# Performance work log

Measured on AMD Instinct MI355X. Metric: run time of the kernel, lower is better.

Reference implementation:

```python
import jax, jax.numpy as jnp
import numpy as np

D = 64          # cfg.D_PAIR
NT = 6          # cfg.N_TORSION_OUT
LN_EPS = 1e-5


def _layernorm(x, g, b):
    # torch LayerNorm computed in float32 then cast back
    x32 = x.astype(jnp.float32)
    m = jnp.mean(x32, axis=-1, keepdims=True)
    v = jnp.var(x32, axis=-1, keepdims=True)
    y = (x32 - m) / jnp.sqrt(v + LN_EPS) * g + b
    return y.astype(x.dtype)


def setup_inputs() -> dict:
    key = jax.random.key(0)
    ks = jax.random.split(key, 16)
    B, L = 2, 512
    s = 0.125  # ~xavier scale for fan 64
    inp = {
        "pair": jax.random.normal(ks[0], (B, L, L, D), jnp.float32),
        "torsion": jax.random.normal(ks[1], (B, L, NT), jnp.float32),
        "ln_g": jnp.ones((D,), jnp.float32),
        "ln_b": jnp.zeros((D,), jnp.float32),
        "Wl": jax.random.normal(ks[2], (D, D), jnp.float32) * s,
        "Wr": jax.random.normal(ks[3], (D, D), jnp.float32) * s,
        "Wlg": jax.random.normal(ks[4], (D, D), jnp.float32) * s,
        "blg": jnp.zeros((D,), jnp.float32),
        "Wrg": jax.random.normal(ks[5], (D, D), jnp.float32) * s,
        "brg": jnp.zeros((D,), jnp.float32),
        "Wog": jax.random.normal(ks[6], (D, D), jnp.float32) * s,
        "bog": jnp.zeros((D,), jnp.float32),
        "Wout": jax.random.normal(ks[7], (D, D), jnp.float32) * s,  # 'final' init is zeros; randomized to exercise math
        "bout": jnp.zeros((D,), jnp.float32),
        "lno_g": jnp.ones((D,), jnp.float32),
        "lno_b": jnp.zeros((D,), jnp.float32),
        "Wt": jax.random.normal(ks[8], (1, NT), jnp.float32) * 0.4,
        "bt": jnp.zeros((1,), jnp.float32),
    }
    return inp


def reference(pair, torsion, ln_g, ln_b, Wl, Wr, Wlg, blg, Wrg, brg,
              Wog, bog, Wout, bout, lno_g, lno_b, Wt, bt):
    B, L, _, d = pair.shape
    z = _layernorm(pair, ln_g, ln_b)                         # [B,L,L,D]
    a = (z @ Wl.T) * jax.nn.sigmoid(z @ Wlg.T + blg)         # left proj * gate
    b = (z @ Wr.T) * jax.nn.sigmoid(z @ Wrg.T + brg)         # right proj * gate
    t_w = jax.nn.sigmoid(torsion @ Wt.T + bt)[..., 0]        # [B,L]
    # outgoing=True branch: tw unsqueezed to [B,1,L,1] then transposed(1,2) -> [B,L,1,1]
    a_w = a * t_w[:, :, None, None]
    x = jnp.einsum('bikd,bjkd->bijd', a_w, b) / (L ** 0.5 + 1e-8)
    g = jax.nn.sigmoid(z @ Wog.T + bog)
    out = (_layernorm(x, lno_g, lno_b) @ Wout.T + bout) * g
    return pair + out
```

## Files before the change

kernel.cpp:

```cpp
#include <hip/hip_runtime.h>
#include <stdint.h>

#define LL 512
#define DD 64

typedef __attribute__((ext_vector_type(8))) short bf16x8;
typedef __attribute__((ext_vector_type(4))) float f32x4;

#define MFMA16(a, b, c) __builtin_amdgcn_mfma_f32_16x16x32_bf16((a), (b), (c), 0, 0, 0)

__device__ __forceinline__ float bf2f(unsigned short u) {
    union { unsigned int i; float f; } v; v.i = ((unsigned int)u) << 16; return v.f;
}
__device__ __forceinline__ unsigned short f2bf(float f) {
    union { float f; unsigned int i; } v; v.f = f;
    unsigned int i = v.i;
    return (unsigned short)((i + 0x7FFFu + ((i >> 16) & 1u)) >> 16);
}
__device__ __forceinline__ float sigm(float x) {
    float d = 1.0f + __expf(-x);
    float y = __builtin_amdgcn_rcpf(d);
    return y * __builtin_fmaf(-d, y, 2.0f);
}

__global__ void prep_w(const float* __restrict__ Wl, const float* __restrict__ Wr,
                       const float* __restrict__ Wlg, const float* __restrict__ Wrg,
                       const float* __restrict__ Wog, const float* __restrict__ Wout,
                       unsigned short* __restrict__ Wcat, unsigned short* __restrict__ WoutB) {
    int t = threadIdx.x + blockIdx.x * blockDim.x;
    int stride = blockDim.x * gridDim.x;
    for (int idx = t; idx < 320 * 64; idx += stride) {
        int row = idx >> 6, col = idx & 63;
        int sec = row >> 6, r = row & 63;
        float v;
        switch (sec) {
            case 0:  v = Wl[r * 64 + col];  break;
            case 1:  v = Wlg[r * 64 + col]; break;
            case 2:  v = Wr[r * 64 + col];  break;
            case 3:  v = Wrg[r * 64 + col]; break;
            default: v = Wog[r * 64 + col]; break;
        }
        Wcat[idx] = f2bf(v);
    }
    for (int idx = t; idx < 64 * 64; idx += stride) WoutB[idx] = f2bf(Wout[idx]);
}

__launch_bounds__(256)
__global__ void k1_proj(const float* __restrict__ pair, const float* __restrict__ torsion,
                        const float* __restrict__ ln_g, const float* __restrict__ ln_b,
                        const float* __restrict__ blg, const float* __restrict__ brg,
                        const float* __restrict__ bog, const float* __restrict__ Wt,
                        const float* __restrict__ bt, const unsigned short* __restrict__ Wcat,
                        unsigned short* __restrict__ At, unsigned short* __restrict__ Bt,
                        unsigned short* __restrict__ G) {
    const int bb = blockIdx.z, irow = blockIdx.y, c0 = blockIdx.x * 128;
    const int t = threadIdx.x, w = t >> 6, lane = t & 63;
    const int rsel = lane & 15, koff = lane >> 4;
    const int col = w * 16 + rsel;
    __shared__ unsigned short zs[128][72];
    __shared__ unsigned short awL[64][132];
    __shared__ unsigned short bL[64][132];

    float tww;
    {
        float acc = bt[0];
        #pragma unroll
        for (int n = 0; n < 6; ++n) acc += torsion[(bb * LL + irow) * 6 + n] * Wt[n];
        tww = sigm(acc);
    }

    bf16x8 wfr[5][2];
    #pragma unroll
    for (int s = 0; s < 5; ++s)
        #pragma unroll
        for (int kh = 0; kh < 2; ++kh)
            wfr[s][kh] = *(const bf16x8*)&Wcat[(size_t)(s * 64 + col) * 64 + kh * 32 + koff * 8];
    const float vblg = blg[col], vbrg = brg[col], vbog = bog[col];

    {
        const int sub = lane & 3, rr = lane >> 2;
        const float4* pr4 = (const float4*)(pair + ((size_t)(bb * LL + irow) * LL + c0) * DD);
        #pragma unroll
        for (int p = 0; p < 2; ++p) {
            const int row = w * 32 + p * 16 + rr;
            float4 x[4];
            #pragma unroll
            for (int q = 0; q < 4; ++q) x[q] = pr4[row * 16 + sub * 4 + q];
            float s = 0.f, s2 = 0.f;
            #pragma unroll
            for (int q = 0; q < 4; ++q) {
                s += x[q].x + x[q].y + x[q].z + x[q].w;
                s2 += x[q].x * x[q].x + x[q].y * x[q].y + x[q].z * x[q].z + x[q].w * x[q].w;
            }
            s += __shfl_xor(s, 1);  s2 += __shfl_xor(s2, 1);
            s += __shfl_xor(s, 2);  s2 += __shfl_xor(s2, 2);
            float m = s * 0.015625f;
            float var = s2 * 0.015625f - m * m;
            float rstd = rsqrtf(var + 1e-5f);
            #pragma unroll
            for (int q = 0; q < 4; ++q) {
                float4 lg4 = ((const float4*)ln_g)[sub * 4 + q];
                float4 lb4 = ((const float4*)ln_b)[sub * 4 + q];
                ushort4 zw;
                zw.x = f2bf((x[q].x - m) * rstd * lg4.x + lb4.x);
                zw.y = f2bf((x[q].y - m) * rstd * lg4.y + lb4.y);
                zw.z = f2bf((x[q].z - m) * rstd * lg4.z + lb4.z);
                zw.w = f2bf((x[q].w - m) * rstd * lg4.w + lb4.w);
                *(ushort4*)&zs[row][sub * 16 + q * 4] = zw;
            }
        }
    }
    __syncthreads();

    ushort4 gk[8];
    #pragma unroll
    for (int mi = 0; mi < 8; ++mi) {
        bf16x8 a0 = *(const bf16x8*)&zs[mi * 16 + rsel][koff * 8];
        bf16x8 a1 = *(const bf16x8*)&zs[mi * 16 + rsel][32 + koff * 8];
        f32x4 pl = {0.f, 0.f, 0.f, 0.f}, plg = pl, pr = pl, prg = pl, pog = pl;
        pl  = MFMA16(a0, wfr[0][0], pl);  pl  = MFMA16(a1, wfr[0][1], pl);
        plg = MFMA16(a0, wfr[1][0], plg); plg = MFMA16(a1, wfr[1][1], plg);
        pr  = MFMA16(a0, wfr[2][0], pr);  pr  = MFMA16(a1, wfr[2][1], pr);
        prg = MFMA16(a0, wfr[3][0], prg); prg = MFMA16(a1, wfr[3][1], prg);
        pog = MFMA16(a0, wfr[4][0], pog); pog = MFMA16(a1, wfr[4][1], pog);

        const int crow = mi * 16 + koff * 4;
        unsigned short aw4[4], bm4[4], g4[4];
        #pragma unroll
        for (int r = 0; r < 4; ++r) {
            float av = pl[r] * sigm(plg[r] + vblg) * tww;
            float bv = pr[r] * sigm(prg[r] + vbrg);
            float gv = sigm(pog[r] + vbog);
            aw4[r] = f2bf(av); bm4[r] = f2bf(bv); g4[r] = f2bf(gv);
        }
        *(ushort4*)&awL[col][crow] = make_ushort4(aw4[0], aw4[1], aw4[2], aw4[3]);
        *(ushort4*)&bL[col][crow]  = make_ushort4(bm4[0], bm4[1], bm4[2], bm4[3]);
        gk[mi] = make_ushort4(g4[0], g4[1], g4[2], g4[3]);
    }
    __syncthreads();

    #pragma unroll
    for (int mi = 0; mi < 8; ++mi) {
        const int rbase = mi * 16 + koff * 4;
        zs[rbase + 0][col] = gk[mi].x;
        zs[rbase + 1][col] = gk[mi].y;
        zs[rbase + 2][col] = gk[mi].z;
        zs[rbase + 3][col] = gk[mi].w;
    }
    __syncthreads();

    #pragma unroll
    for (int it = 0; it < 8; ++it) {
        int d = it * 8 + (t >> 5);
        int c8 = (t & 31) * 4;
        size_t base = ((size_t)(bb * 64 + d) * LL + irow) * LL + c0 + c8;
        *(ushort4*)&At[base] = *(const ushort4*)&awL[d][c8];
        *(ushort4*)&Bt[base] = *(const ushort4*)&bL[d][c8];
    }
    #pragma unroll
    for (int it = 0; it < 8; ++it) {
        int r = it * 16 + (t >> 4), cc = (t & 15) * 4;
        size_t pos = (size_t)(bb * LL + irow) * LL + c0 + r;
        *(ushort4*)&G[pos * DD + cc] = *(const ushort4*)&zs[r][cc];
    }
}

__launch_bounds__(256, 2)
__global__ void k2_gemm(const unsigned short* __restrict__ At,
                        const unsigned short* __restrict__ Bt,
                        unsigned short* __restrict__ Xt) {
    int lin = blockIdx.x + (blockIdx.y << 4);
    int nlin = (lin & 7) * 256 + (lin >> 3);
    const int p = nlin >> 4;
    const int tile = nlin & 15;
    const int i0 = (tile >> 2) * 128, j0 = (tile & 3) * 128;
    const int t = threadIdx.x, lane = t & 63, w = t >> 6;
    const int wm = w >> 1, wn = w & 1;
    const int rsel = lane & 15, koff = lane >> 4;
    __shared__ unsigned short Cs[128][136];

    f32x4 acc[4][4];
    #pragma unroll
    for (int i = 0; i < 4; ++i)
        #pragma unroll
        for (int j = 0; j < 4; ++j) acc[i][j] = (f32x4){0.f, 0.f, 0.f, 0.f};

    const unsigned short* ap =
        At + (size_t)p * LL * LL + (size_t)(i0 + wm * 64 + rsel) * LL + koff * 8;
    const unsigned short* bp =
        Bt + (size_t)p * LL * LL + (size_t)(j0 + wn * 64 + rsel) * LL + koff * 8;

    for (int k0 = 0; k0 < LL; k0 += 32) {
        bf16x8 af[4], bfr[4];
        #pragma unroll
        for (int mi = 0; mi < 4; ++mi)
            af[mi] = *(const bf16x8*)(ap + (size_t)mi * 16 * LL + k0);
        #pragma unroll
        for (int ni = 0; ni < 4; ++ni)
            bfr[ni] = *(const bf16x8*)(bp + (size_t)ni * 16 * LL + k0);
        #pragma unroll
        for (int mi = 0; mi < 4; ++mi)
            #pragma unroll
            for (int ni = 0; ni < 4; ++ni)
                acc[mi][ni] = MFMA16(af[mi], bfr[ni], acc[mi][ni]);
    }

    const float s = 1.0f / (sqrtf((float)LL) + 1e-8f);
    #pragma unroll
    for (int mi = 0; mi < 4; ++mi)
        #pragma unroll
        for (int ni = 0; ni < 4; ++ni)
            #pragma unroll
            for (int r = 0; r < 4; ++r)
                Cs[wm * 64 + mi * 16 + koff * 4 + r][wn * 64 + ni * 16 + rsel] =
                    f2bf(acc[mi][ni][r] * s);
    __syncthreads();
    #pragma unroll
    for (int it = 0; it < 8; ++it) {
        int row = it * 16 + (t >> 4), colc = (t & 15) * 8;
        uint4 v = *(const uint4*)&Cs[row][colc];
        *(uint4*)&Xt[((size_t)p * LL + i0 + row) * LL + j0 + colc] = v;
    }
}

__launch_bounds__(256)
__global__ void k3_out(const unsigned short* __restrict__ Xt, const unsigned short* __restrict__ G,
                       const float* __restrict__ pairIn, const unsigned short* __restrict__ WoutB,
                       const float* __restrict__ lno_g, const float* __restrict__ lno_b,
                       const float* __restrict__ bout, float* __restrict__ out) {
    const int bb = blockIdx.z, irow = blockIdx.y, c0 = blockIdx.x * 128;
    const int t = threadIdx.x, w = t >> 6, lane = t & 63;
    __shared__ unsigned short x1[64][128];
    __shared__ unsigned short x2[128][72];

    #pragma unroll
    for (int q = 0; q < 4; ++q) {
        int idx = t + q * 256, d = idx >> 4, c8 = idx & 15;
        uint4 v = *(const uint4*)&Xt[((size_t)(bb * 64 + d) * LL + irow) * LL + c0 + c8 * 8];
        *(uint4*)&x1[d][c8 * 8] = v;
    }
    __syncthreads();
    {
        const int c = t & 127, half = t >> 7;
        unsigned short tmp[32];
        #pragma unroll
        for (int dd = 0; dd < 32; ++dd) tmp[dd] = x1[half * 32 + dd][c];
        #pragma unroll
        for (int q = 0; q < 4; ++q)
            *(uint4*)&x2[c][half * 32 + q * 8] = *(const uint4*)&tmp[q * 8];
    }
    __syncthreads();

    {
        const int sub = lane & 3, rr = lane >> 2;
        #pragma unroll
        for (int p = 0; p < 2; ++p) {
            const int row = w * 32 + p * 16 + rr;
            ushort4 raw[4];
            #pragma unroll
            for (int q = 0; q < 4; ++q) raw[q] = *(const ushort4*)&x2[row][sub * 16 + q * 4];
            float xv[16];
            #pragma unroll
            for (int q = 0; q < 4; ++q) {
                xv[q * 4 + 0] = bf2f(raw[q].x);
                xv[q * 4 + 1] = bf2f(raw[q].y);
                xv[q * 4 + 2] = bf2f(raw[q].z);
                xv[q * 4 + 3] = bf2f(raw[q].w);
            }
            float s = 0.f, s2 = 0.f;
            #pragma unroll
            for (int e = 0; e < 16; ++e) { s += xv[e]; s2 += xv[e] * xv[e]; }
            s += __shfl_xor(s, 1);  s2 += __shfl_xor(s2, 1);
            s += __shfl_xor(s, 2);  s2 += __shfl_xor(s2, 2);
            float m = s * 0.015625f;
            float var = s2 * 0.015625f - m * m;
            float rstd = rsqrtf(var + 1e-5f);
            #pragma unroll
            for (int q = 0; q < 4; ++q) {
                float4 lg4 = ((const float4*)lno_g)[sub * 4 + q];
                float4 lb4 = ((const float4*)lno_b)[sub * 4 + q];
                ushort4 zw;
                zw.x = f2bf((xv[q * 4 + 0] - m) * rstd * lg4.x + lb4.x);
                zw.y = f2bf((xv[q * 4 + 1] - m) * rstd * lg4.y + lb4.y);
                zw.z = f2bf((xv[q * 4 + 2] - m) * rstd * lg4.z + lb4.z);
                zw.w = f2bf((xv[q * 4 + 3] - m) * rstd * lg4.w + lb4.w);
                *(ushort4*)&x2[row][sub * 16 + q * 4] = zw;
            }
        }
    }
    __syncthreads();

    unsigned short* o_lds = &x1[0][0];
    const int rsel = lane & 15, koff = lane >> 4;
    #pragma unroll
    for (int mh = 0; mh < 2; ++mh) {
        const int mi = 2 * w + mh;
        bf16x8 a0 = *(const bf16x8*)&x2[mi * 16 + rsel][koff * 8];
        bf16x8 a1 = *(const bf16x8*)&x2[mi * 16 + rsel][32 + koff * 8];
        #pragma unroll
        for (int n = 0; n < 4; ++n) {
            f32x4 pacc = {0.f, 0.f, 0.f, 0.f};
            const unsigned short* wrow = WoutB + (size_t)(n * 16 + rsel) * 64;
            pacc = MFMA16(a0, *(const bf16x8*)&wrow[koff * 8], pacc);
            pacc = MFMA16(a1, *(const bf16x8*)&wrow[32 + koff * 8], pacc);
            const float bo = bout[n * 16 + rsel];
            #pragma unroll
            for (int r = 0; r < 4; ++r)
                o_lds[(mi * 16 + koff * 4 + r) * 64 + n * 16 + rsel] = f2bf(pacc[r] + bo);
        }
    }
    __syncthreads();

    #pragma unroll
    for (int q = 0; q < 4; ++q) {
        int e = q * 2048 + t * 8;
        int c = e >> 6, o = e & 63;
        size_t pos = (size_t)(bb * LL + irow) * LL + c0 + c;
        uint4 ov = *(const uint4*)&o_lds[c * 64 + o];
        uint4 gv = *(const uint4*)&G[pos * DD + o];
        const unsigned short* ovp = (const unsigned short*)&ov;
        const unsigned short* gvp = (const unsigned short*)&gv;
        float4 p0 = *(const float4*)&pairIn[pos * DD + o];
        float4 p1 = *(const float4*)&pairIn[pos * DD + o + 4];
        float4 r0, r1;
        r0.x = p0.x + bf2f(ovp[0]) * bf2f(gvp[0]);
        r0.y = p0.y + bf2f(ovp[1]) * bf2f(gvp[1]);
        r0.z = p0.z + bf2f(ovp[2]) * bf2f(gvp[2]);
        r0.w = p0.w + bf2f(ovp[3]) * bf2f(gvp[3]);
        r1.x = p1.x + bf2f(ovp[4]) * bf2f(gvp[4]);
        r1.y = p1.y + bf2f(ovp[5]) * bf2f(gvp[5]);
        r1.z = p1.z + bf2f(ovp[6]) * bf2f(gvp[6]);
        r1.w = p1.w + bf2f(ovp[7]) * bf2f(gvp[7]);
        *(float4*)&out[pos * DD + o] = r0;
        *(float4*)&out[pos * DD + o + 4] = r1;
    }
}

extern "C" void kernel_launch(void* const* d_in, const int* in_sizes, int n_in,
                              void* d_out, int out_size, void* d_ws, size_t ws_size,
                              hipStream_t stream) {
    const float* pair    = (const float*)d_in[0];
    const float* torsion = (const float*)d_in[1];
    const float* ln_g    = (const float*)d_in[2];
    const float* ln_b    = (const float*)d_in[3];
    const float* Wl      = (const float*)d_in[4];
    const float* Wr      = (const float*)d_in[5];
    const float* Wlg     = (const float*)d_in[6];
    const float* blg     = (const float*)d_in[7];
    const float* Wrg     = (const float*)d_in[8];
    const float* brg     = (const float*)d_in[9];
    const float* Wog     = (const float*)d_in[10];
    const float* bog     = (const float*)d_in[11];
    const float* Wout    = (const float*)d_in[12];
    const float* bout    = (const float*)d_in[13];
    const float* lno_g   = (const float*)d_in[14];
    const float* lno_b   = (const float*)d_in[15];
    const float* Wt      = (const float*)d_in[16];
    const float* bt      = (const float*)d_in[17];
    float* outp = (float*)d_out;

    const size_t PLANE_B = (size_t)128 * LL * LL * 2;
    const size_t need = 4 * PLANE_B + (320 * 64 + 64 * 64) * 2;
    if (ws_size < need) return;

    char* ws = (char*)d_ws;
    unsigned short* At    = (unsigned short*)(ws);
    unsigned short* Bt_   = (unsigned short*)(ws + PLANE_B);
    unsigned short* G     = (unsigned short*)(ws + 2 * PLANE_B);
    unsigned short* Xt    = (unsigned short*)(ws + 3 * PLANE_B);
    unsigned short* Wcat  = (unsigned short*)(ws + 4 * PLANE_B);
    unsigned short* WoutB = Wcat + 320 * 64;

    prep_w<<<dim3(40), dim3(256), 0, stream>>>(Wl, Wr, Wlg, Wrg, Wog, Wout, Wcat, WoutB);
    k1_proj<<<dim3(4, LL, 2), dim3(256), 0, stream>>>(pair, torsion, ln_g, ln_b, blg, brg,
                                                      bog, Wt, bt, Wcat, At, Bt_, G);
    k2_gemm<<<dim3(16, 128), dim3(256), 0, stream>>>(At, Bt_, Xt);
    k3_out<<<dim3(4, LL, 2), dim3(256), 0, stream>>>(Xt, G, pair, WoutB, lno_g, lno_b, bout, outp);
}
```

Baseline: 297.6 us.

## Store projection outputs in MFMA-fragment-packed layout for contiguous GEMM loads

Result: faster. 260.5 us (median of 3 runs) (-12.5%).

```diff
diff --git a/kernel.cpp b/kernel.cpp
--- a/kernel.cpp
+++ b/kernel.cpp
@@ -51,22 +51,27 @@
                         const float* __restrict__ blg, const float* __restrict__ brg,
                         const float* __restrict__ bog, const float* __restrict__ Wt,
                         const float* __restrict__ bt, const unsigned short* __restrict__ Wcat,
-                        unsigned short* __restrict__ At, unsigned short* __restrict__ Bt,
+                        unsigned short* __restrict__ At2, unsigned short* __restrict__ Bt2,
                         unsigned short* __restrict__ G) {
-    const int bb = blockIdx.z, irow = blockIdx.y, c0 = blockIdx.x * 128;
+    const int cj = blockIdx.x;
+    const int a  = blockIdx.y;
+    const int bb = blockIdx.z;
+    const int c0j = cj * 32;
     const int t = threadIdx.x, w = t >> 6, lane = t & 63;
     const int rsel = lane & 15, koff = lane >> 4;
     const int col = w * 16 + rsel;
     __shared__ unsigned short zs[128][72];
-    __shared__ unsigned short awL[64][132];
-    __shared__ unsigned short bL[64][132];
-
-    float tww;
-    {
+    __shared__ unsigned short awL[64][136];
+    __shared__ unsigned short bL[64][136];
+
+    float tw4[4];
+    #pragma unroll
+    for (int il = 0; il < 4; ++il) {
         float acc = bt[0];
         #pragma unroll
-        for (int n = 0; n < 6; ++n) acc += torsion[(bb * LL + irow) * 6 + n] * Wt[n];
-        tww = sigm(acc);
+        for (int n = 0; n < 6; ++n)
+            acc += torsion[((size_t)(bb * LL + 4 * a + il)) * 6 + n] * Wt[n];
+        tw4[il] = sigm(acc);
     }
 
     bf16x8 wfr[5][2];
@@ -79,13 +84,14 @@
 
     {
         const int sub = lane & 3, rr = lane >> 2;
-        const float4* pr4 = (const float4*)(pair + ((size_t)(bb * LL + irow) * LL + c0) * DD);
+        const float4* pr4 = (const float4*)(pair +
+            (((size_t)(bb * LL + 4 * a + w) * LL) + c0j) * DD);
         #pragma unroll
         for (int p = 0; p < 2; ++p) {
-            const int row = w * 32 + p * 16 + rr;
+            const int rl = p * 16 + rr;
             float4 x[4];
             #pragma unroll
-            for (int q = 0; q < 4; ++q) x[q] = pr4[row * 16 + sub * 4 + q];
+            for (int q = 0; q < 4; ++q) x[q] = pr4[rl * 16 + sub * 4 + q];
             float s = 0.f, s2 = 0.f;
             #pragma unroll
             for (int q = 0; q < 4; ++q) {
@@ -106,7 +112,7 @@
                 zw.y = f2bf((x[q].y - m) * rstd * lg4.y + lb4.y);
                 zw.z = f2bf((x[q].z - m) * rstd * lg4.z + lb4.z);
                 zw.w = f2bf((x[q].w - m) * rstd * lg4.w + lb4.w);
-                *(ushort4*)&zs[row][sub * 16 + q * 4] = zw;
+                *(ushort4*)&zs[w * 32 + rl][sub * 16 + q * 4] = zw;
             }
         }
     }
@@ -124,6 +130,7 @@
         prg = MFMA16(a0, wfr[3][0], prg); prg = MFMA16(a1, wfr[3][1], prg);
         pog = MFMA16(a0, wfr[4][0], pog); pog = MFMA16(a1, wfr[4][1], pog);
 
+        const float tww = tw4[mi >> 1];
         const int crow = mi * 16 + koff * 4;
         unsigned short aw4[4], bm4[4], g4[4];
         #pragma unroll
@@ -149,34 +156,43 @@
     }
     __syncthreads();
 
-    #pragma unroll
-    for (int it = 0; it < 8; ++it) {
-        int d = it * 8 + (t >> 5);
-        int c8 = (t & 31) * 4;
-        size_t base = ((size_t)(bb * 64 + d) * LL + irow) * LL + c0 + c8;
-        *(ushort4*)&At[base] = *(const ushort4*)&awL[d][c8];
-        *(ushort4*)&Bt[base] = *(const ushort4*)&bL[d][c8];
-    }
-    #pragma unroll
-    for (int it = 0; it < 8; ++it) {
-        int r = it * 16 + (t >> 4), cc = (t & 15) * 4;
-        size_t pos = (size_t)(bb * LL + irow) * LL + c0 + r;
+    const int itb = a >> 5;
+    const int wmb = (a >> 4) & 1;
+    const int mif = (a >> 2) & 3;
+    const int ri0 = (a & 3) * 4;
+    {
+        const int il = t & 3, g = (t >> 2) & 3, dlow = t >> 4;
+        const int lfrag = g * 16 + ri0 + il;
+        #pragma unroll
+        for (int q = 0; q < 4; ++q) {
+            const int d = q * 16 + dlow;
+            const int p = bb * 64 + d;
+            size_t base = (((size_t)(p * 4 + itb) * 16 + cj) * 4096)
+                        + wmb * 2048 + mif * 512 + (size_t)lfrag * 8;
+            *(uint4*)&At2[base] = *(const uint4*)&awL[d][il * 32 + g * 8];
+            *(uint4*)&Bt2[base] = *(const uint4*)&bL[d][il * 32 + g * 8];
+        }
+    }
+    #pragma unroll
+    for (int it8 = 0; it8 < 8; ++it8) {
+        int r = it8 * 16 + (t >> 4), cc = (t & 15) * 4;
+        size_t pos = ((size_t)(bb * LL + 4 * a + (r >> 5)) * LL) + c0j + (r & 31);
         *(ushort4*)&G[pos * DD + cc] = *(const ushort4*)&zs[r][cc];
     }
 }
 
-__launch_bounds__(256, 2)
-__global__ void k2_gemm(const unsigned short* __restrict__ At,
-                        const unsigned short* __restrict__ Bt,
+__launch_bounds__(256, 4)
+__global__ void k2_gemm(const unsigned short* __restrict__ At2,
+                        const unsigned short* __restrict__ Bt2,
                         unsigned short* __restrict__ Xt) {
     int lin = blockIdx.x + (blockIdx.y << 4);
     int nlin = (lin & 7) * 256 + (lin >> 3);
     const int p = nlin >> 4;
     const int tile = nlin & 15;
-    const int i0 = (tile >> 2) * 128, j0 = (tile & 3) * 128;
+    const int it = tile >> 2, jt = tile & 3;
+    const int i0 = it * 128, j0 = jt * 128;
     const int t = threadIdx.x, lane = t & 63, w = t >> 6;
     const int wm = w >> 1, wn = w & 1;
-    const int rsel = lane & 15, koff = lane >> 4;
     __shared__ unsigned short Cs[128][136];
 
     f32x4 acc[4][4];
@@ -185,19 +201,20 @@
         #pragma unroll
         for (int j = 0; j < 4; ++j) acc[i][j] = (f32x4){0.f, 0.f, 0.f, 0.f};
 
-    const unsigned short* ap =
-        At + (size_t)p * LL * LL + (size_t)(i0 + wm * 64 + rsel) * LL + koff * 8;
-    const unsigned short* bp =
-        Bt + (size_t)p * LL * LL + (size_t)(j0 + wn * 64 + rsel) * LL + koff * 8;
-
-    for (int k0 = 0; k0 < LL; k0 += 32) {
+    const unsigned short* ap = At2 + ((size_t)(p * 4 + it) * 16) * 4096
+                             + wm * 2048 + lane * 8;
+    const unsigned short* bp = Bt2 + ((size_t)(p * 4 + jt) * 16) * 4096
+                             + wn * 2048 + lane * 8;
+
+    #pragma unroll 4
+    for (int k = 0; k < 16; ++k) {
         bf16x8 af[4], bfr[4];
         #pragma unroll
         for (int mi = 0; mi < 4; ++mi)
-            af[mi] = *(const bf16x8*)(ap + (size_t)mi * 16 * LL + k0);
+            af[mi] = *(const bf16x8*)(ap + (size_t)k * 4096 + mi * 512);
         #pragma unroll
         for (int ni = 0; ni < 4; ++ni)
-            bfr[ni] = *(const bf16x8*)(bp + (size_t)ni * 16 * LL + k0);
+            bfr[ni] = *(const bf16x8*)(bp + (size_t)k * 4096 + ni * 512);
         #pragma unroll
         for (int mi = 0; mi < 4; ++mi)
             #pragma unroll
@@ -205,6 +222,7 @@
                 acc[mi][ni] = MFMA16(af[mi], bfr[ni], acc[mi][ni]);
     }
 
+    const int rsel = lane & 15, koff = lane >> 4;
     const float s = 1.0f / (sqrtf((float)LL) + 1e-8f);
     #pragma unroll
     for (int mi = 0; mi < 4; ++mi)
@@ -216,8 +234,8 @@
                     f2bf(acc[mi][ni][r] * s);
     __syncthreads();
     #pragma unroll
-    for (int it = 0; it < 8; ++it) {
-        int row = it * 16 + (t >> 4), colc = (t & 15) * 8;
+    for (int it8 = 0; it8 < 8; ++it8) {
+        int row = it8 * 16 + (t >> 4), colc = (t & 15) * 8;
         uint4 v = *(const uint4*)&Cs[row][colc];
         *(uint4*)&Xt[((size_t)p * LL + i0 + row) * LL + j0 + colc] = v;
     }
@@ -364,16 +382,16 @@
     if (ws_size < need) return;
 
     char* ws = (char*)d_ws;
-    unsigned short* At    = (unsigned short*)(ws);
-    unsigned short* Bt_   = (unsigned short*)(ws + PLANE_B);
+    unsigned short* At2   = (unsigned short*)(ws);
+    unsigned short* Bt2   = (unsigned short*)(ws + PLANE_B);
     unsigned short* G     = (unsigned short*)(ws + 2 * PLANE_B);
     unsigned short* Xt    = (unsigned short*)(ws + 3 * PLANE_B);
     unsigned short* Wcat  = (unsigned short*)(ws + 4 * PLANE_B);
     unsigned short* WoutB = Wcat + 320 * 64;
 
     prep_w<<<dim3(40), dim3(256), 0, stream>>>(Wl, Wr, Wlg, Wrg, Wog, Wout, Wcat, WoutB);
-    k1_proj<<<dim3(4, LL, 2), dim3(256), 0, stream>>>(pair, torsion, ln_g, ln_b, blg, brg,
-                                                      bog, Wt, bt, Wcat, At, Bt_, G);
-    k2_gemm<<<dim3(16, 128), dim3(256), 0, stream>>>(At, Bt_, Xt);
+    k1_proj<<<dim3(16, 128, 2), dim3(256), 0, stream>>>(pair, torsion, ln_g, ln_b, blg, brg,
+                                                        bog, Wt, bt, Wcat, At2, Bt2, G);
+    k2_gemm<<<dim3(16, 128), dim3(256), 0, stream>>>(At2, Bt2, Xt);
     k3_out<<<dim3(4, LL, 2), dim3(256), 0, stream>>>(Xt, G, pair, WoutB, lno_g, lno_b, bout, outp);
 }
```
